# Optimization experiments

Measured on AMD Instinct MI355X. Metric: run time of the kernel, lower is better.

Reference implementation:

```python
import jax, jax.numpy as jnp
import numpy as np

KH, KW = 3, 3  # spatial kernel from kernel_size=(1,3,3,C)


def _extract_patches_valid(x, kh, kw):
    # TF extract_image_patches ordering: depth = (row, col, channel) flattened.
    B, H, W, C = x.shape
    Ho, Wo = H - kh + 1, W - kw + 1
    # stack kh*kw shifted views -> [B, Ho, Wo, kh*kw, C]
    views = [x[:, i:i + Ho, j:j + Wo, :] for i in range(kh) for j in range(kw)]
    patches = jnp.stack(views, axis=3)
    return patches.reshape(B, Ho, Wo, kh * kw * C)


def setup_inputs() -> dict:
    key = jax.random.key(0)
    k1, k2, k3 = jax.random.split(key, 3)
    B, H, W, C = 32, 112, 112, 32
    filters = 128
    patch_dim = KH * KW * C  # 288
    x = jax.random.normal(k1, (B, H, W, C), dtype=jnp.float32)
    ccs = jax.random.uniform(k2, (patch_dim, filters), dtype=jnp.float32)  # RandomUniform(0,1)
    beta = jax.random.uniform(k3, (filters,), dtype=jnp.float32)
    return {"x": x, "ccs": ccs, "beta": beta}


def reference(x, ccs, beta):
    B = x.shape[0]
    patch_dim, filters = ccs.shape
    patches = _extract_patches_valid(x, KH, KW)  # [B, Ho, Wo, patch_dim]
    Ho, Wo = patches.shape[1], patches.shape[2]
    p = patches.reshape(B, Ho * Wo, patch_dim)  # [B, P, D]
    # squared distance: ||p||^2 - 2 p.ccs + ||ccs||^2  -> [B, P, filters]
    p_sq = jnp.sum(p * p, axis=2, keepdims=True)
    c_sq = jnp.sum(ccs * ccs, axis=0, keepdims=True)
    scores = p_sq - 2.0 * jnp.einsum('bpd,df->bpf', p, ccs) + c_sq
    out = jnp.exp(-beta * scores)  # RBF activation, beta broadcast over filters
    return out.reshape(B, Ho, Wo, filters)
```

## Files before the change

kernel.cpp:

```cpp
#include <hip/hip_runtime.h>


typedef __attribute__((ext_vector_type(8))) short bf16x8;
typedef __attribute__((ext_vector_type(4))) float f32x4;

#define HH 112
#define WW 112
#define CC 32
#define HO 110
#define WO 110
#define NF 128
#define KD 288
#define RPX 114
#define XP 32
#define CSP 116

__device__ __forceinline__ unsigned short f32_to_bf16(float f) {
    unsigned u = __float_as_uint(f);
    unsigned r = u + 0x7FFFu + ((u >> 16) & 1u);
    return (unsigned short)(r >> 16);
}

__global__ __launch_bounds__(256) void rbf_prologue(const float* __restrict__ ccs,
                                                    unsigned short* __restrict__ ccs_t,
                                                    float* __restrict__ c_sq) {
    int idx = blockIdx.x * 256 + threadIdx.x;
    int d = idx >> 7;
    int f = idx & 127;
    ccs_t[f * KD + d] = f32_to_bf16(ccs[idx]);
    if (blockIdx.x == 0 && threadIdx.x < 128) {
        const int fc = threadIdx.x;
        float s = 0.f;
        #pragma unroll 8
        for (int dd = 0; dd < KD; ++dd) {
            float v = ccs[dd * NF + fc];
            s += v * v;
        }
        c_sq[fc] = s;
    }
}

__global__ __launch_bounds__(256) void rbf_main(const float* __restrict__ x,
                                                const unsigned short* __restrict__ ccs_t,
                                                const float* __restrict__ c_sq,
                                                const float* __restrict__ beta,
                                                float* __restrict__ out) {
    __shared__ unsigned short xs[3 * RPX * XP];
    __shared__ float colsum[3 * CSP];
    __shared__ float p_sq[112];

    const int t = threadIdx.x;
    const int y0 = blockIdx.x;
    const int b  = blockIdx.y;

    const int lane  = t & 63;
    const int wave  = t >> 6;
    const int laneM = lane & 15;
    const int quad  = lane >> 4;
    const int pl    = laneM & 1;

    #pragma unroll
    for (int p = 0; p < 11; ++p) {
        int idx = t + p * 256;
        if (idx < 3 * 112 * 8) {
            int q = idx & 7;
            int ic = idx >> 3;
            int col = ic % 112;
            int i = ic / 112;
            const float4 v = *(const float4*)(x + ((size_t)(b * HH + y0 + i) * WW + col) * CC + q * 4);
            unsigned short h0 = f32_to_bf16(v.x), h1 = f32_to_bf16(v.y);
            unsigned short h2 = f32_to_bf16(v.z), h3 = f32_to_bf16(v.w);
            uint2 pk;
            pk.x = (unsigned)h0 | ((unsigned)h1 << 16);
            pk.y = (unsigned)h2 | ((unsigned)h3 << 16);
            *(uint2*)(&xs[(i * RPX + col) * XP + q * 4]) = pk;
            float part = v.x * v.x + v.y * v.y + v.z * v.z + v.w * v.w;
            part += __shfl_xor(part, 1);
            part += __shfl_xor(part, 2);
            part += __shfl_xor(part, 4);
            if (q == 0) colsum[i * CSP + col] = part;
        }
    }
    __syncthreads();

    if (t < 112) {
        float s = 0.f;
        #pragma unroll
        for (int i = 0; i < 3; ++i)
            #pragma unroll
            for (int j = 0; j < 3; ++j)
                s += colsum[i * CSP + t + j];
        p_sq[t] = s;
    }
    __syncthreads();

    const unsigned short* ap0 = ccs_t + (size_t)(wave * 32 + laneM) * KD + quad * 8;
    const unsigned short* ap1 = ap0 + 16 * KD;

    const int fb = wave * 32 + quad * 4;
    const float4 cs0 = *(const float4*)(c_sq + fb);
    const float4 cs1 = *(const float4*)(c_sq + fb + 16);
    const float4 bt0 = *(const float4*)(beta + fb);
    const float4 bt1 = *(const float4*)(beta + fb + 16);

    f32x4 acc[7][2];
    #pragma unroll
    for (int mi = 0; mi < 7; ++mi) {
        acc[mi][0] = (f32x4){0.f, 0.f, 0.f, 0.f};
        acc[mi][1] = (f32x4){0.f, 0.f, 0.f, 0.f};
    }

    #pragma unroll
    for (int kb = 0; kb < 9; ++kb) {
        const int ki = kb / 3, kj = kb % 3;
        bf16x8 a0 = *(const bf16x8*)(ap0 + kb * 32);
        bf16x8 a1 = *(const bf16x8*)(ap1 + kb * 32);
        #pragma unroll
        for (int mi = 0; mi < 7; ++mi) {
            const bf16x8 bf = *(const bf16x8*)(&xs[(ki * RPX + mi * 16 + laneM + kj) * XP + quad * 8]);
            acc[mi][0] = __builtin_amdgcn_mfma_f32_16x16x32_bf16(a0, bf, acc[mi][0], 0, 0, 0);
            acc[mi][1] = __builtin_amdgcn_mfma_f32_16x16x32_bf16(a1, bf, acc[mi][1], 0, 0, 0);
        }
    }

    float* orow = out + (size_t)((b * HO + y0) * WO) * NF;
    #pragma unroll
    for (int mi = 0; mi < 7; ++mi) {
        const int px = mi * 16 + laneM;
        const float ps = p_sq[px];
        f32x4 o0, o1;
        o0[0] = __expf(-bt0.x * (ps - 2.f * acc[mi][0][0] + cs0.x));
        o0[1] = __expf(-bt0.y * (ps - 2.f * acc[mi][0][1] + cs0.y));
        o0[2] = __expf(-bt0.z * (ps - 2.f * acc[mi][0][2] + cs0.z));
        o0[3] = __expf(-bt0.w * (ps - 2.f * acc[mi][0][3] + cs0.w));
        o1[0] = __expf(-bt1.x * (ps - 2.f * acc[mi][1][0] + cs1.x));
        o1[1] = __expf(-bt1.y * (ps - 2.f * acc[mi][1][1] + cs1.y));
        o1[2] = __expf(-bt1.z * (ps - 2.f * acc[mi][1][2] + cs1.z));
        o1[3] = __expf(-bt1.w * (ps - 2.f * acc[mi][1][3] + cs1.w));

        f32x4 sendv = pl ? o0 : o1;
        f32x4 recv;
        recv[0] = __shfl_xor(sendv[0], 1);
        recv[1] = __shfl_xor(sendv[1], 1);
        recv[2] = __shfl_xor(sendv[2], 1);
        recv[3] = __shfl_xor(sendv[3], 1);
        const f32x4 v1 = pl ? recv : o0;
        const f32x4 v2 = pl ? o1 : recv;

        const int pxe = mi * 16 + (laneM & ~1);
        float* op1 = orow + (size_t)pxe * NF + fb + pl * 16;
        if (pxe < WO)
            __builtin_nontemporal_store(v1, (f32x4*)op1);
        if (pxe + 1 < WO)
            __builtin_nontemporal_store(v2, (f32x4*)(op1 + NF));
    }
}

extern "C" void kernel_launch(void* const* d_in, const int* in_sizes, int n_in,
                              void* d_out, int out_size, void* d_ws, size_t ws_size,
                              hipStream_t stream) {
    const float* x    = (const float*)d_in[0];
    const float* ccs  = (const float*)d_in[1];
    const float* beta = (const float*)d_in[2];
    float* out = (float*)d_out;

    unsigned short* ccs_t = (unsigned short*)d_ws;
    float* c_sq = (float*)((char*)d_ws + 128 * KD * sizeof(unsigned short));

    rbf_prologue<<<144, 256, 0, stream>>>(ccs, ccs_t, c_sq);
    rbf_main<<<dim3(110, 32), 256, 0, stream>>>(x, ccs_t, c_sq, beta, out);
}
```

Baseline: 275.9 us.

## Tile main kernel into two-row, 56-column blocks to reuse input halo rows

Each block now computes two output rows over half the width instead of one full row, keeping the same grid size. It stages four input rows of 58 columns in shared memory, so each staged input row serves more output rows and the x read amplification drops. Smaller shared-memory and accumulator footprints should allow more resident waves per CU. In exchange, each 56-column half is covered by four 16-pixel MFMA tiles, so a slightly larger share of the matrix work is thrown away.

```diff
diff --git a/kernel.cpp b/kernel.cpp
--- a/kernel.cpp
+++ b/kernel.cpp
@@ -11,9 +11,12 @@
 #define WO 110
 #define NF 128
 #define KD 288
-#define RPX 114
+#define RPXC 58
 #define XP 32
-#define CSP 116
+#define CSPC 60
+#define ORPB 2
+#define SROWS 4
+#define OCOL 56
 
 __device__ __forceinline__ unsigned short f32_to_bf16(float f) {
     unsigned u = __float_as_uint(f);
@@ -45,12 +48,15 @@
                                                 const float* __restrict__ c_sq,
                                                 const float* __restrict__ beta,
                                                 float* __restrict__ out) {
-    __shared__ unsigned short xs[3 * RPX * XP];
-    __shared__ float colsum[3 * CSP];
-    __shared__ float p_sq[112];
+    __shared__ unsigned short xs[(SROWS * RPXC + 8) * XP];
+    __shared__ float colsum[SROWS * CSPC + 8];
+    __shared__ float p_sq[ORPB * 64];
 
     const int t = threadIdx.x;
-    const int y0 = blockIdx.x;
+    const int strip = blockIdx.x >> 1;
+    const int cb    = blockIdx.x & 1;
+    const int y0 = strip * ORPB;
+    const int x0 = cb * OCOL;
     const int b  = blockIdx.y;
 
     const int lane  = t & 63;
@@ -60,36 +66,39 @@
     const int pl    = laneM & 1;
 
     #pragma unroll
-    for (int p = 0; p < 11; ++p) {
+    for (int p = 0; p < 8; ++p) {
         int idx = t + p * 256;
-        if (idx < 3 * 112 * 8) {
+        if (idx < SROWS * RPXC * 8) {
             int q = idx & 7;
             int ic = idx >> 3;
-            int col = ic % 112;
-            int i = ic / 112;
-            const float4 v = *(const float4*)(x + ((size_t)(b * HH + y0 + i) * WW + col) * CC + q * 4);
+            int col = ic % RPXC;
+            int i = ic / RPXC;
+            int cg = x0 + col; if (cg > WW - 1) cg = WW - 1;
+            const float4 v = *(const float4*)(x + ((size_t)(b * HH + y0 + i) * WW + cg) * CC + q * 4);
             unsigned short h0 = f32_to_bf16(v.x), h1 = f32_to_bf16(v.y);
             unsigned short h2 = f32_to_bf16(v.z), h3 = f32_to_bf16(v.w);
             uint2 pk;
             pk.x = (unsigned)h0 | ((unsigned)h1 << 16);
             pk.y = (unsigned)h2 | ((unsigned)h3 << 16);
-            *(uint2*)(&xs[(i * RPX + col) * XP + q * 4]) = pk;
+            *(uint2*)(&xs[(i * RPXC + col) * XP + q * 4]) = pk;
             float part = v.x * v.x + v.y * v.y + v.z * v.z + v.w * v.w;
             part += __shfl_xor(part, 1);
             part += __shfl_xor(part, 2);
             part += __shfl_xor(part, 4);
-            if (q == 0) colsum[i * CSP + col] = part;
+            if (q == 0) colsum[i * CSPC + col] = part;
         }
     }
     __syncthreads();
 
-    if (t < 112) {
+    if (t < ORPB * 64) {
+        int r = t >> 6;
+        int c = t & 63;
         float s = 0.f;
         #pragma unroll
         for (int i = 0; i < 3; ++i)
             #pragma unroll
             for (int j = 0; j < 3; ++j)
-                s += colsum[i * CSP + t + j];
+                s += colsum[(r + i) * CSPC + c + j];
         p_sq[t] = s;
     }
     __syncthreads();
@@ -103,56 +112,59 @@
     const float4 bt0 = *(const float4*)(beta + fb);
     const float4 bt1 = *(const float4*)(beta + fb + 16);
 
-    f32x4 acc[7][2];
-    #pragma unroll
-    for (int mi = 0; mi < 7; ++mi) {
-        acc[mi][0] = (f32x4){0.f, 0.f, 0.f, 0.f};
-        acc[mi][1] = (f32x4){0.f, 0.f, 0.f, 0.f};
-    }
+    for (int r = 0; r < ORPB; ++r) {
+        f32x4 acc[4][2];
+        #pragma unroll
+        for (int mi = 0; mi < 4; ++mi) {
+            acc[mi][0] = (f32x4){0.f, 0.f, 0.f, 0.f};
+            acc[mi][1] = (f32x4){0.f, 0.f, 0.f, 0.f};
+        }
 
-    #pragma unroll
-    for (int kb = 0; kb < 9; ++kb) {
-        const int ki = kb / 3, kj = kb % 3;
-        bf16x8 a0 = *(const bf16x8*)(ap0 + kb * 32);
-        bf16x8 a1 = *(const bf16x8*)(ap1 + kb * 32);
         #pragma unroll
-        for (int mi = 0; mi < 7; ++mi) {
-            const bf16x8 bf = *(const bf16x8*)(&xs[(ki * RPX + mi * 16 + laneM + kj) * XP + quad * 8]);
-            acc[mi][0] = __builtin_amdgcn_mfma_f32_16x16x32_bf16(a0, bf, acc[mi][0], 0, 0, 0);
-            acc[mi][1] = __builtin_amdgcn_mfma_f32_16x16x32_bf16(a1, bf, acc[mi][1], 0, 0, 0);
+        for (int kb = 0; kb < 9; ++kb) {
+            const int ki = kb / 3, kj = kb % 3;
+            bf16x8 a0 = *(const bf16x8*)(ap0 + kb * 32);
+            bf16x8 a1 = *(const bf16x8*)(ap1 + kb * 32);
+            #pragma unroll
+            for (int mi = 0; mi < 4; ++mi) {
+                const bf16x8 bf = *(const bf16x8*)(&xs[((r + ki) * RPXC + mi * 16 + laneM + kj) * XP + quad * 8]);
+                acc[mi][0] = __builtin_amdgcn_mfma_f32_16x16x32_bf16(a0, bf, acc[mi][0], 0, 0, 0);
+                acc[mi][1] = __builtin_amdgcn_mfma_f32_16x16x32_bf16(a1, bf, acc[mi][1], 0, 0, 0);
+            }
         }
-    }
 
-    float* orow = out + (size_t)((b * HO + y0) * WO) * NF;
-    #pragma unroll
-    for (int mi = 0; mi < 7; ++mi) {
-        const int px = mi * 16 + laneM;
-        const float ps = p_sq[px];
-        f32x4 o0, o1;
-        o0[0] = __expf(-bt0.x * (ps - 2.f * acc[mi][0][0] + cs0.x));
-        o0[1] = __expf(-bt0.y * (ps - 2.f * acc[mi][0][1] + cs0.y));
-        o0[2] = __expf(-bt0.z * (ps - 2.f * acc[mi][0][2] + cs0.z));
-        o0[3] = __expf(-bt0.w * (ps - 2.f * acc[mi][0][3] + cs0.w));
-        o1[0] = __expf(-bt1.x * (ps - 2.f * acc[mi][1][0] + cs1.x));
-        o1[1] = __expf(-bt1.y * (ps - 2.f * acc[mi][1][1] + cs1.y));
-        o1[2] = __expf(-bt1.z * (ps - 2.f * acc[mi][1][2] + cs1.z));
-        o1[3] = __expf(-bt1.w * (ps - 2.f * acc[mi][1][3] + cs1.w));
+        float* orow = out + (size_t)((b * HO + y0 + r) * WO) * NF;
+        #pragma unroll
+        for (int mi = 0; mi < 4; ++mi) {
+            const int px = mi * 16 + laneM;
+            const float ps = p_sq[r * 64 + px];
+            f32x4 o0, o1;
+            o0[0] = __expf(-bt0.x * (ps - 2.f * acc[mi][0][0] + cs0.x));
+            o0[1] = __expf(-bt0.y * (ps - 2.f * acc[mi][0][1] + cs0.y));
+            o0[2] = __expf(-bt0.z * (ps - 2.f * acc[mi][0][2] + cs0.z));
+            o0[3] = __expf(-bt0.w * (ps - 2.f * acc[mi][0][3] + cs0.w));
+            o1[0] = __expf(-bt1.x * (ps - 2.f * acc[mi][1][0] + cs1.x));
+            o1[1] = __expf(-bt1.y * (ps - 2.f * acc[mi][1][1] + cs1.y));
+            o1[2] = __expf(-bt1.z * (ps - 2.f * acc[mi][1][2] + cs1.z));
+            o1[3] = __expf(-bt1.w * (ps - 2.f * acc[mi][1][3] + cs1.w));
 
-        f32x4 sendv = pl ? o0 : o1;
-        f32x4 recv;
-        recv[0] = __shfl_xor(sendv[0], 1);
-        recv[1] = __shfl_xor(sendv[1], 1);
-        recv[2] = __shfl_xor(sendv[2], 1);
-        recv[3] = __shfl_xor(sendv[3], 1);
-        const f32x4 v1 = pl ? recv : o0;
-        const f32x4 v2 = pl ? o1 : recv;
+            f32x4 sendv = pl ? o0 : o1;
+            f32x4 recv;
+            recv[0] = __shfl_xor(sendv[0], 1);
+            recv[1] = __shfl_xor(sendv[1], 1);
+            recv[2] = __shfl_xor(sendv[2], 1);
+            recv[3] = __shfl_xor(sendv[3], 1);
+            const f32x4 v1 = pl ? recv : o0;
+            const f32x4 v2 = pl ? o1 : recv;
 
-        const int pxe = mi * 16 + (laneM & ~1);
-        float* op1 = orow + (size_t)pxe * NF + fb + pl * 16;
-        if (pxe < WO)
-            __builtin_nontemporal_store(v1, (f32x4*)op1);
-        if (pxe + 1 < WO)
-            __builtin_nontemporal_store(v2, (f32x4*)(op1 + NF));
+            const int pxe = mi * 16 + (laneM & ~1);
+            const int gpxe = x0 + pxe;
+            float* op1 = orow + (size_t)gpxe * NF + fb + pl * 16;
+            if (pxe < OCOL && gpxe < WO)
+                __builtin_nontemporal_store(v1, (f32x4*)op1);
+            if (pxe < OCOL && gpxe + 1 < WO)
+                __builtin_nontemporal_store(v2, (f32x4*)(op1 + NF));
+        }
     }
 }
 
```

After: 285.1 us. 3.3% more time.
